# Optimization experiments

Hardware: AMD Instinct MI355X
Metric: run time of the kernel (lower is better)

The kernel has to match this reference:

```python
import jax, jax.numpy as jnp
import numpy as np

N, E = 50000, 250000          # nodes, edges
IN, OUT, EDIM = 9, 84, 1      # NNConv(9, 84), edge nn Linear(1, 9*84)
EPS = 1e-5                    # BatchNorm1d default eps


def setup_inputs() -> dict:
    key = jax.random.key(0)
    ks = jax.random.split(key, 8)
    return {
        "x": jax.random.normal(ks[0], (N, IN), jnp.float32),
        "edge_index": jax.random.randint(ks[1], (2, E), 0, N, dtype=jnp.int64),
        "edge_attr": jax.random.normal(ks[2], (E, EDIM), jnp.float32),
        # edge nn: Linear(EDIM, IN*OUT) generating per-edge weight matrices
        "nn_w": jax.random.normal(ks[3], (EDIM, IN * OUT), jnp.float32) * (1.0 / np.sqrt(EDIM)),
        "nn_b": jnp.zeros((IN * OUT,), jnp.float32),
        # NNConv root weight + bias
        "root": jax.random.normal(ks[4], (IN, OUT), jnp.float32) * (1.0 / np.sqrt(IN)),
        "bias": jnp.zeros((OUT,), jnp.float32),
        # BatchNorm1d(84) affine params
        "gamma": jnp.ones((OUT,), jnp.float32),
        "beta": jnp.zeros((OUT,), jnp.float32),
    }


def reference(x, edge_index, edge_attr, nn_w, nn_b, root, bias, gamma, beta):
    src, dst = edge_index[0], edge_index[1]
    # per-edge weight matrices: [E, IN, OUT]
    w_e = (edge_attr @ nn_w + nn_b).reshape(E, IN, OUT)
    # gather source node features and apply edge-specific matmul: [E, OUT]
    msg = jnp.einsum('ei,eio->eo', x[src], w_e)
    # scatter-add to destination nodes (NNConv default aggr='add'): [N, OUT]
    aggr = jax.ops.segment_sum(msg, dst, num_segments=N)
    out = x @ root + aggr + bias
    # BatchNorm1d(84), training mode (biased batch stats)
    mean = out.mean(0)
    var = out.var(0)
    out = (out - mean) * jax.lax.rsqrt(var + EPS) * gamma + beta
    return out
```

## Files before the change

### kernel.cpp

```cpp
#include <hip/hip_runtime.h>

#define N_NODES 50000
#define E_EDGES 250000
#define IN_F 9
#define OUT_F 84
#define GROUPS 21
#define BN_EPS 1e-5f

#define NB_TILE 24
#define NTILES ((N_NODES + NB_TILE - 1) / NB_TILE)
#define NCOPIES 32
#define CAP 32

#define VDIM 27
#define NPAIR 378
#define NM 405
#define SLEN 408

#define CNT_OFF   0
#define STATC_OFF 50048
#define SLOT_OFF  63232
#define S_OFF     3263232

__global__ void fill_slots_kernel(const int* __restrict__ ei,
                                  const float* __restrict__ ea,
                                  int* __restrict__ cnt,
                                  int2* __restrict__ slot,
                                  float* __restrict__ statc) {
    if (blockIdx.x == 0) {
        for (int t = threadIdx.x; t < NCOPIES * SLEN; t += blockDim.x)
            statc[t] = 0.0f;
    }
    int e = blockIdx.x * blockDim.x + threadIdx.x;
    if (e < E_EDGES) {
        int dst = ei[E_EDGES + e];
        int pos = atomicAdd(&cnt[dst], 1);
        if (pos < CAP)
            slot[dst * CAP + pos] = make_int2(ei[e], __float_as_int(ea[e]));
    }
}

__global__ void gather_gram_kernel(const float* __restrict__ x,
                                   const int*   __restrict__ cnt,
                                   const int2*  __restrict__ slot,
                                   float* __restrict__ S,
                                   float* __restrict__ statc) {
    __shared__ float V[VDIM * (NB_TILE + 1)];
    __shared__ unsigned char pI[NPAIR], pJ[NPAIR];

    const int tid = threadIdx.x;

    for (int t = tid; t < NPAIR; t += blockDim.x) {
        int tt = t, i = 0;
        while (tt >= VDIM - i) { tt -= VDIM - i; ++i; }
        pI[t] = (unsigned char)i;
        pJ[t] = (unsigned char)(i + tt);
    }

    const int nbase = blockIdx.x * NB_TILE;

    if (tid < NB_TILE * IN_F) {
        int nl = tid / IN_F, i = tid - nl * IN_F;
        int n = nbase + nl;
        float xv = 0.f, s0 = 0.f, s1 = 0.f;
        if (n < N_NODES) {
            xv = x[n * IN_F + i];
            int c = cnt[n];
            if (c > CAP) c = CAP;
            const int2* row = &slot[n * CAP];
            int k = 0;
            for (; k + 2 <= c; k += 2) {
                int2 r0 = row[k], r1 = row[k + 1];
                float a0 = x[r0.x * IN_F + i];
                float a1 = x[r1.x * IN_F + i];
                s0 += a0 + a1;
                s1 += __int_as_float(r0.y) * a0 + __int_as_float(r1.y) * a1;
            }
            if (k < c) {
                int2 r0 = row[k];
                float a0 = x[r0.x * IN_F + i];
                s0 += a0;
                s1 += __int_as_float(r0.y) * a0;
            }
            S[n * 18 + i]     = s0;
            S[n * 18 + 9 + i] = s1;
        }
        V[i * (NB_TILE + 1) + nl]            = xv;
        V[(9 + i) * (NB_TILE + 1) + nl]      = s0;
        V[(18 + i) * (NB_TILE + 1) + nl]     = s1;
    }
    __syncthreads();

    float* sc = statc + (blockIdx.x & (NCOPIES - 1)) * SLEN;
    for (int t = tid; t < NM; t += blockDim.x) {
        float acc = 0.f;
        if (t < NPAIR) {
            const float* vi = &V[pI[t] * (NB_TILE + 1)];
            const float* vj = &V[pJ[t] * (NB_TILE + 1)];
#pragma unroll
            for (int n = 0; n < NB_TILE; ++n) acc += vi[n] * vj[n];
        } else {
            const float* vi = &V[(t - NPAIR) * (NB_TILE + 1)];
#pragma unroll
            for (int n = 0; n < NB_TILE; ++n) acc += vi[n];
        }
        atomicAdd(&sc[t], acc);
    }
}

__global__ void final_kernel(const float* __restrict__ x,
                             const float* __restrict__ S,
                             const float* __restrict__ nw,
                             const float* __restrict__ nb,
                             const float* __restrict__ root,
                             const float* __restrict__ bias,
                             const float* __restrict__ gamma,
                             const float* __restrict__ beta,
                             const float* __restrict__ statc,
                             float* __restrict__ out) {
    __shared__ __align__(16) float4 Ws[IN_F * GROUPS];
    __shared__ __align__(16) float4 Bs[IN_F * GROUPS];
    __shared__ __align__(16) float4 Rs[IN_F * GROUPS];
    __shared__ __align__(16) float4 bs4[GROUPS];
    __shared__ float M[NM];
    __shared__ __align__(16) float scale[OUT_F];
    __shared__ __align__(16) float shift[OUT_F];
    __shared__ float Xt[NB_TILE * IN_F];
    __shared__ float St[NB_TILE * 18];

    const int tid = threadIdx.x;
    const int nbase = blockIdx.x * NB_TILE;

    for (int t = tid; t < IN_F * GROUPS; t += blockDim.x) {
        Ws[t] = ((const float4*)nw)[t];
        Bs[t] = ((const float4*)nb)[t];
        Rs[t] = ((const float4*)root)[t];
    }
    if (tid < GROUPS) bs4[tid] = ((const float4*)bias)[tid];

    if (tid < NB_TILE * IN_F) {
        int nl = tid / IN_F, i = tid - nl * IN_F;
        int n = nbase + nl;
        float xv = 0.f, s0 = 0.f, s1 = 0.f;
        if (n < N_NODES) {
            xv = x[n * IN_F + i];
            s0 = S[n * 18 + i];
            s1 = S[n * 18 + 9 + i];
        }
        Xt[nl * IN_F + i]  = xv;
        St[nl * 18 + i]     = s0;
        St[nl * 18 + 9 + i] = s1;
    }

    for (int t = tid; t < NM; t += blockDim.x) {
        float a = 0.f;
#pragma unroll
        for (int c = 0; c < NCOPIES; ++c) a += statc[c * SLEN + t];
        M[t] = a;
    }
    __syncthreads();

    if (tid < OUT_F) {
        const int o = tid;
        float c[VDIM];
#pragma unroll
        for (int i = 0; i < IN_F; ++i) {
            c[i]      = root[i * OUT_F + o];
            c[9 + i]  = nb[i * OUT_F + o];
            c[18 + i] = nw[i * OUT_F + o];
        }
        float sv = 0.f;
#pragma unroll
        for (int i = 0; i < VDIM; ++i) sv += M[NPAIR + i] * c[i];
        float q = 0.f;
        int t2 = 0;
        for (int i = 0; i < VDIM; ++i) {
            q += c[i] * c[i] * M[t2++];
            for (int j = i + 1; j < VDIM; ++j)
                q += 2.f * c[i] * c[j] * M[t2++];
        }
        const float b = bias[o];
        const float inv_n = 1.0f / (float)N_NODES;
        float mean  = (sv + (float)N_NODES * b) * inv_n;
        float sumsq = q + 2.f * b * sv + (float)N_NODES * b * b;
        float var   = sumsq * inv_n - mean * mean;
        float sc    = rsqrtf(var + BN_EPS) * gamma[o];
        scale[o] = sc;
        shift[o] = beta[o] - mean * sc;
    }
    __syncthreads();

    const int g = tid % GROUPS;
    if (tid < 252) {
        float4 sc4 = *(const float4*)&scale[g * 4];
        float4 sh4 = *(const float4*)&shift[g * 4];
#pragma unroll
        for (int k = 0; k < 2; ++k) {
            int p  = tid + k * 252;
            int nl = p / GROUPS;
            int n  = nbase + nl;
            if (n < N_NODES) {
                float4 acc = bs4[g];
#pragma unroll
                for (int i = 0; i < IN_F; ++i) {
                    float xv = Xt[nl * IN_F + i];
                    float s0 = St[nl * 18 + i];
                    float s1 = St[nl * 18 + 9 + i];
                    float4 r = Rs[i * GROUPS + g];
                    float4 w = Ws[i * GROUPS + g];
                    float4 b = Bs[i * GROUPS + g];
                    acc.x += xv * r.x + s1 * w.x + s0 * b.x;
                    acc.y += xv * r.y + s1 * w.y + s0 * b.y;
                    acc.z += xv * r.z + s1 * w.z + s0 * b.z;
                    acc.w += xv * r.w + s1 * w.w + s0 * b.w;
                }
                acc.x = acc.x * sc4.x + sh4.x;
                acc.y = acc.y * sc4.y + sh4.y;
                acc.z = acc.z * sc4.z + sh4.z;
                acc.w = acc.w * sc4.w + sh4.w;
                *(float4*)&out[n * OUT_F + g * 4] = acc;
            }
        }
    }
}

extern "C" void kernel_launch(void* const* d_in, const int* in_sizes, int n_in,
                              void* d_out, int out_size, void* d_ws, size_t ws_size,
                              hipStream_t stream) {
    const float* x     = (const float*)d_in[0];
    const int*   ei    = (const int*)d_in[1];
    const float* ea    = (const float*)d_in[2];
    const float* nw    = (const float*)d_in[3];
    const float* nb    = (const float*)d_in[4];
    const float* root  = (const float*)d_in[5];
    const float* bias  = (const float*)d_in[6];
    const float* gamma = (const float*)d_in[7];
    const float* beta  = (const float*)d_in[8];
    float*       out   = (float*)d_out;

    float* wsf   = (float*)d_ws;
    int*   wsi   = (int*)d_ws;
    int*   cnt   = wsi + CNT_OFF;
    float* statc = wsf + STATC_OFF;
    int2*  slot  = (int2*)(wsi + SLOT_OFF);
    float* S     = wsf + S_OFF;

    hipMemsetAsync(cnt, 0, N_NODES * sizeof(int), stream);
    fill_slots_kernel<<<(E_EDGES + 255) / 256, 256, 0, stream>>>(ei, ea, cnt, slot, statc);
    gather_gram_kernel<<<NTILES, 256, 0, stream>>>(x, cnt, slot, S, statc);
    final_kernel<<<NTILES, 256, 0, stream>>>(x, S, nw, nb, root, bias,
                                             gamma, beta, statc, out);
}
```

Baseline: 124.8 us.

## Double node tile, stage edge slots in shared memory, read weights from LDS

Doubles the node tile per block from 24 to 48 and halves the grid. Each block now copies its nodes' edge slot records into shared memory with vectorized int4 loads before the gather, and unrolls the neighbour loop by four. The per-channel BN coefficient setup reads root, edge-nn and bias values from already staged LDS instead of global memory. This cuts per-block overhead and the number of statistics atomics, at the cost of more shared memory and fewer blocks, which may lower occupancy.

New measurement: 122.2 us. 1.02x faster.

```diff
diff --git a/kernel.cpp b/kernel.cpp
--- a/kernel.cpp
+++ b/kernel.cpp
@@ -7,7 +7,7 @@
 #define GROUPS 21
 #define BN_EPS 1e-5f
 
-#define NB_TILE 24
+#define NB_TILE 48
 #define NTILES ((N_NODES + NB_TILE - 1) / NB_TILE)
 #define NCOPIES 32
 #define CAP 32
@@ -46,9 +46,12 @@
                                    float* __restrict__ S,
                                    float* __restrict__ statc) {
     __shared__ float V[VDIM * (NB_TILE + 1)];
+    __shared__ __align__(16) int2 rec[NB_TILE][CAP];
+    __shared__ int cnt_s[NB_TILE];
     __shared__ unsigned char pI[NPAIR], pJ[NPAIR];
 
     const int tid = threadIdx.x;
+    const int nbase = blockIdx.x * NB_TILE;
 
     for (int t = tid; t < NPAIR; t += blockDim.x) {
         int tt = t, i = 0;
@@ -56,28 +59,47 @@
         pI[t] = (unsigned char)i;
         pJ[t] = (unsigned char)(i + tt);
     }
-
-    const int nbase = blockIdx.x * NB_TILE;
-
-    if (tid < NB_TILE * IN_F) {
-        int nl = tid / IN_F, i = tid - nl * IN_F;
+    if (tid < NB_TILE) {
+        int n = nbase + tid;
+        int c = (n < N_NODES) ? cnt[n] : 0;
+        cnt_s[tid] = (c > CAP) ? CAP : c;
+    }
+    __syncthreads();
+
+    if (tid < NB_TILE * 4) {
+        int nl = tid >> 2, part = tid & 3;
+        int c = cnt_s[nl];
+        const int4* grow = (const int4*)&slot[(nbase + nl) * CAP];
+        int4* lrow = (int4*)&rec[nl][0];
+#pragma unroll
+        for (int j = 0; j < 4; ++j) {
+            int s = part * 8 + j * 2;
+            if (s < c) lrow[part * 4 + j] = grow[part * 4 + j];
+        }
+    }
+    __syncthreads();
+
+    for (int it = tid; it < NB_TILE * IN_F; it += blockDim.x) {
+        int nl = it / IN_F, i = it - nl * IN_F;
         int n = nbase + nl;
         float xv = 0.f, s0 = 0.f, s1 = 0.f;
         if (n < N_NODES) {
             xv = x[n * IN_F + i];
-            int c = cnt[n];
-            if (c > CAP) c = CAP;
-            const int2* row = &slot[n * CAP];
+            int c = cnt_s[nl];
+            const int2* r = rec[nl];
             int k = 0;
-            for (; k + 2 <= c; k += 2) {
-                int2 r0 = row[k], r1 = row[k + 1];
+            for (; k + 4 <= c; k += 4) {
+                int2 r0 = r[k], r1 = r[k+1], r2 = r[k+2], r3 = r[k+3];
                 float a0 = x[r0.x * IN_F + i];
                 float a1 = x[r1.x * IN_F + i];
-                s0 += a0 + a1;
-                s1 += __int_as_float(r0.y) * a0 + __int_as_float(r1.y) * a1;
+                float a2 = x[r2.x * IN_F + i];
+                float a3 = x[r3.x * IN_F + i];
+                s0 += (a0 + a1) + (a2 + a3);
+                s1 += __int_as_float(r0.y) * a0 + __int_as_float(r1.y) * a1
+                    + __int_as_float(r2.y) * a2 + __int_as_float(r3.y) * a3;
             }
-            if (k < c) {
-                int2 r0 = row[k];
+            for (; k < c; ++k) {
+                int2 r0 = r[k];
                 float a0 = x[r0.x * IN_F + i];
                 s0 += a0;
                 s1 += __int_as_float(r0.y) * a0;
@@ -85,9 +107,9 @@
             S[n * 18 + i]     = s0;
             S[n * 18 + 9 + i] = s1;
         }
-        V[i * (NB_TILE + 1) + nl]            = xv;
-        V[(9 + i) * (NB_TILE + 1) + nl]      = s0;
-        V[(18 + i) * (NB_TILE + 1) + nl]     = s1;
+        V[i * (NB_TILE + 1) + nl]        = xv;
+        V[(9 + i) * (NB_TILE + 1) + nl]  = s0;
+        V[(18 + i) * (NB_TILE + 1) + nl] = s1;
     }
     __syncthreads();
 
@@ -138,8 +160,8 @@
     }
     if (tid < GROUPS) bs4[tid] = ((const float4*)bias)[tid];
 
-    if (tid < NB_TILE * IN_F) {
-        int nl = tid / IN_F, i = tid - nl * IN_F;
+    for (int it = tid; it < NB_TILE * IN_F; it += blockDim.x) {
+        int nl = it / IN_F, i = it - nl * IN_F;
         int n = nbase + nl;
         float xv = 0.f, s0 = 0.f, s1 = 0.f;
         if (n < N_NODES) {
@@ -147,7 +169,7 @@
             s0 = S[n * 18 + i];
             s1 = S[n * 18 + 9 + i];
         }
-        Xt[nl * IN_F + i]  = xv;
+        Xt[nl * IN_F + i]   = xv;
         St[nl * 18 + i]     = s0;
         St[nl * 18 + 9 + i] = s1;
     }
@@ -161,13 +183,13 @@
     __syncthreads();
 
     if (tid < OUT_F) {
-        const int o = tid;
+        const int o = tid, g4 = o >> 2, cm = o & 3;
         float c[VDIM];
 #pragma unroll
         for (int i = 0; i < IN_F; ++i) {
-            c[i]      = root[i * OUT_F + o];
-            c[9 + i]  = nb[i * OUT_F + o];
-            c[18 + i] = nw[i * OUT_F + o];
+            c[i]      = ((const float*)&Rs[i * GROUPS + g4])[cm];
+            c[9 + i]  = ((const float*)&Bs[i * GROUPS + g4])[cm];
+            c[18 + i] = ((const float*)&Ws[i * GROUPS + g4])[cm];
         }
         float sv = 0.f;
 #pragma unroll
@@ -179,7 +201,7 @@
             for (int j = i + 1; j < VDIM; ++j)
                 q += 2.f * c[i] * c[j] * M[t2++];
         }
-        const float b = bias[o];
+        const float b = ((const float*)&bs4[g4])[cm];
         const float inv_n = 1.0f / (float)N_NODES;
         float mean  = (sv + (float)N_NODES * b) * inv_n;
         float sumsq = q + 2.f * b * sv + (float)N_NODES * b * b;
@@ -195,7 +217,7 @@
         float4 sc4 = *(const float4*)&scale[g * 4];
         float4 sh4 = *(const float4*)&shift[g * 4];
 #pragma unroll
-        for (int k = 0; k < 2; ++k) {
+        for (int k = 0; k < 4; ++k) {
             int p  = tid + k * 252;
             int nl = p / GROUPS;
             int n  = nbase + nl;
```
